# Kernel optimization log

Measured on AMD Instinct MI355X. Metric: run time of the kernel, lower is better.

## Reference

```python
import jax, jax.numpy as jnp
import numpy as np

B, C, N, K, COUT = 8, 128, 10000, 16, 256


def setup_inputs() -> dict:
    key = jax.random.key(0)
    ks = jax.random.split(key, 8)
    x = jax.random.normal(ks[0], (B, C, N, 1), dtype=jnp.float32)
    edge_index = jax.random.randint(ks[1], (2, B, N, K), 0, N)
    s1 = 1.0 / np.sqrt(C)
    W1 = jax.random.uniform(ks[2], (C, C), jnp.float32, -s1, s1)   # nn1 1x1 conv weight
    b1 = jax.random.uniform(ks[3], (C,), jnp.float32, -s1, s1)
    Wp = jax.random.uniform(ks[4], (C, C), jnp.float32, -s1, s1)   # nn_pooling Linear
    bp = jax.random.uniform(ks[5], (C,), jnp.float32, -s1, s1)
    s2 = 1.0 / np.sqrt(2 * C)
    W2 = jax.random.uniform(ks[6], (COUT, 2 * C), jnp.float32, -s2, s2)  # nn2 1x1 conv
    b2 = jax.random.uniform(ks[7], (COUT,), jnp.float32, -s2, s2)
    return dict(x=x, edge_index=edge_index, W1=W1, b1=b1, Wp=Wp, bp=bp, W2=W2, b2=b2)


def reference(x, edge_index, W1, b1, Wp, bp, W2, b2):
    b, c, n, _ = x.shape
    k = edge_index.shape[-1]
    # nn1: 1x1 conv (channel mix) + ReLU -> [B,C,N,1]
    h = jax.nn.relu(jnp.einsum('bcns,dc->bdns', x, W1) + b1[None, :, None, None])
    # batched_index_select: gather neighbor features along vertex dim -> [B,C,N,K]
    hn = h[:, :, :, 0]                              # [B,C,N]
    idx = edge_index[0].reshape(b, 1, n * k)        # broadcast over C
    xj = jnp.take_along_axis(hn, idx, axis=2).reshape(b, c, n, k)
    # nn_pooling: Linear over channel dim + ReLU (transpose(1,3) in torch == act on C)
    xj = jax.nn.relu(jnp.einsum('bcnk,dc->bdnk', xj, Wp) + bp[None, :, None, None])
    # max-pool over neighbors, keepdim -> [B,C,N,1]
    xj = jnp.max(xj, axis=-1, keepdims=True)
    # concat along channels, nn2: 1x1 conv + ReLU -> [B,COUT,N,1]
    cat = jnp.concatenate([h, xj], axis=1)
    out = jax.nn.relu(jnp.einsum('bcns,dc->bdns', cat, W2) + b2[None, :, None, None])
    return out
```

## Files before the change

### kernel.cpp

```cpp
#include <hip/hip_runtime.h>

#define NODES 10000
#define BATCH 8
#define CH    128
#define KNB   16
#define CO    256

typedef __bf16 bf16x8 __attribute__((ext_vector_type(8)));
typedef float  f32x4  __attribute__((ext_vector_type(4)));

__device__ __forceinline__ unsigned short f2bf(float f) {
  unsigned u = __float_as_uint(f);
  u = (u + 0x7FFFu + ((u >> 16) & 1u)) >> 16;
  return (unsigned short)u;
}

__device__ __forceinline__ unsigned pkmax(unsigned a, unsigned b) {
  unsigned d;
  asm("v_pk_max_u16 %0, %1, %2" : "=v"(d) : "v"(a), "v"(b));
  return d;
}
__device__ __forceinline__ uint4 pkmax4(uint4 a, uint4 b) {
  a.x = pkmax(a.x, b.x); a.y = pkmax(a.y, b.y);
  a.z = pkmax(a.z, b.z); a.w = pkmax(a.w, b.w);
  return a;
}
__device__ __forceinline__ bf16x8 asbf8(uint4 u) {
  union { uint4 u; bf16x8 b; } c; c.u = u; return c.b;
}

__device__ __forceinline__ void gload_lds16(const void* g, void* l) {
  __builtin_amdgcn_global_load_lds(
      (const __attribute__((address_space(1))) unsigned int*)g,
      (__attribute__((address_space(3))) unsigned int*)l, 16, 0, 0);
}

__device__ __forceinline__ void lds_barrier() {
  asm volatile("s_waitcnt lgkmcnt(0)" ::: "memory");
  __builtin_amdgcn_sched_barrier(0);
  __builtin_amdgcn_s_barrier();
}

__global__ __launch_bounds__(256) void prep(
    const float* __restrict__ W1, const float* __restrict__ Wp,
    const float* __restrict__ W2,
    unsigned short* __restrict__ W1b, unsigned short* __restrict__ Wpb,
    unsigned short* __restrict__ W2b)
{
  int i = blockIdx.x * 256 + threadIdx.x;
  const float* src; unsigned short* dst; int off;
  if (i < 4096)      { src = W1; dst = W1b; off = i; }
  else if (i < 8192) { src = Wp; dst = Wpb; off = i - 4096; }
  else               { src = W2; dst = W2b; off = i - 8192; }
  float4 v = ((const float4*)src)[off];
  ushort4 o;
  o.x = f2bf(v.x); o.y = f2bf(v.y); o.z = f2bf(v.z); o.w = f2bf(v.w);
  ((ushort4*)dst)[off] = o;
}

__global__ __launch_bounds__(256) void prep_x(
    const float* __restrict__ x, unsigned short* __restrict__ x_t)
{
  const int b  = blockIdx.y;
  const int n0 = blockIdx.x * 64;
  const int t  = threadIdx.x;
  const size_t nb = (size_t)b * NODES;

  __shared__ __align__(16) unsigned short Bt[64 * 128];
  char* BtB = (char*)Bt;

  const float* X = x + (size_t)b * CH * NODES;
#pragma unroll
  for (int rep = 0; rep < 4; ++rep) {
    int flat = t + rep * 256;
    int c2 = flat >> 4, n4 = flat & 15;
    int c  = c2 * 2;
    int gn = n0 + n4 * 4;
    float4 a0 = make_float4(0.f,0.f,0.f,0.f), a1 = a0;
    if (gn < NODES) {
      a0 = *(const float4*)(X + (size_t)c * NODES + gn);
      a1 = *(const float4*)(X + (size_t)(c + 1) * NODES + gn);
    }
    float v0[4] = {a0.x, a0.y, a0.z, a0.w};
    float v1[4] = {a1.x, a1.y, a1.z, a1.w};
#pragma unroll
    for (int i = 0; i < 4; ++i) {
      int nn = n4 * 4 + i;
      unsigned pk = (unsigned)f2bf(v0[i]) | ((unsigned)f2bf(v1[i]) << 16);
      int phys = nn * 256 + (((c2 >> 2) ^ (nn & 7)) << 4) + ((c2 & 3) << 2);
      *(unsigned*)(BtB + phys) = pk;
    }
  }
  __syncthreads();

  {
    int nl = t >> 2;
    int gn = n0 + nl;
#pragma unroll
    for (int rep = 0; rep < 4; ++rep) {
      int g = (t & 3) + rep * 4;
      int phys = nl * 256 + ((g ^ (nl & 7)) << 4);
      uint4 v = *(const uint4*)(BtB + phys);
      if (gn < NODES)
        *(uint4*)((char*)x_t + (nb + (size_t)gn) * 256 + g * 16) = v;
    }
  }
}

__device__ __forceinline__ void hz_stage(
    unsigned short* buf, const unsigned short* __restrict__ x_t,
    size_t nb, int n0, int w, int lane)
{
#pragma unroll
  for (int rep = 0; rep < 4; ++rep) {
    const int row0 = w * 16 + rep * 4;
    const int nl = row0 + (lane >> 4);
    const int c  = lane & 15;
    const int l  = c ^ (nl & 7);
    int gn = n0 + nl; if (gn > NODES - 1) gn = NODES - 1;
    const unsigned short* src = x_t + (nb + (size_t)gn) * CH + l * 8;
    gload_lds16(src, (char*)buf + row0 * 256);
  }
  __builtin_amdgcn_sched_barrier(0);
}

__device__ __forceinline__ void hz_compute(
    const unsigned short* buf, unsigned short* Ht, unsigned short* Zt,
    const uint4 (&af)[4][4], const uint4 (&af2)[4][4],
    const float* __restrict__ b1, const float* __restrict__ bp,
    unsigned short* __restrict__ h_t, unsigned short* __restrict__ z_t,
    size_t nb, int n0, int t, int w, int lm, int q)
{
  const char* BtB = (const char*)buf;
  char* HtB = (char*)Ht;
  char* ZtB = (char*)Zt;
  const int d0  = (w & 1) * 64;
  const int nbw = (w >> 1) * 32;

  f32x4 acc[4][2];
#pragma unroll
  for (int dt = 0; dt < 4; ++dt)
#pragma unroll
    for (int nt = 0; nt < 2; ++nt) acc[dt][nt] = (f32x4){0.f,0.f,0.f,0.f};

#pragma unroll
  for (int kt = 0; kt < 4; ++kt)
#pragma unroll
    for (int nt = 0; nt < 2; ++nt) {
      int nl = nbw + nt * 16 + lm;
      int chunk = kt * 4 + q;
      int phys = nl * 256 + ((chunk ^ (nl & 7)) << 4);
      bf16x8 bb = asbf8(*(const uint4*)(BtB + phys));
#pragma unroll
      for (int dt = 0; dt < 4; ++dt)
        acc[dt][nt] = __builtin_amdgcn_mfma_f32_16x16x32_bf16(
            asbf8(af[dt][kt]), bb, acc[dt][nt], 0, 0, 0);
    }

#pragma unroll
  for (int dt = 0; dt < 4; ++dt) {
    int dbase = d0 + dt * 16 + q * 4;
    float4 bi = *(const float4*)(b1 + dbase);
    float bv[4] = {bi.x, bi.y, bi.z, bi.w};
#pragma unroll
    for (int nt = 0; nt < 2; ++nt) {
      int nl = nbw + nt * 16 + lm;
      ushort4 o;
      o.x = f2bf(fmaxf(acc[dt][nt][0] + bv[0], 0.f));
      o.y = f2bf(fmaxf(acc[dt][nt][1] + bv[1], 0.f));
      o.z = f2bf(fmaxf(acc[dt][nt][2] + bv[2], 0.f));
      o.w = f2bf(fmaxf(acc[dt][nt][3] + bv[3], 0.f));
      int chunk = dbase >> 3;
      int phys  = nl * 256 + ((chunk ^ (nl & 7)) << 4) + ((q & 1) << 3);
      *(ushort4*)(HtB + phys) = o;
    }
  }

  lds_barrier();

  {
    int nl = t >> 2;
    int gn = n0 + nl;
#pragma unroll
    for (int rep = 0; rep < 4; ++rep) {
      int g = (t & 3) + rep * 4;
      int phys = nl * 256 + ((g ^ (nl & 7)) << 4);
      uint4 v = *(const uint4*)(HtB + phys);
      if (gn < NODES)
        *(uint4*)((char*)h_t + (nb + (size_t)gn) * 256 + g * 16) = v;
    }
  }

#pragma unroll
  for (int dt = 0; dt < 4; ++dt)
#pragma unroll
    for (int nt = 0; nt < 2; ++nt) acc[dt][nt] = (f32x4){0.f,0.f,0.f,0.f};

#pragma unroll
  for (int kt = 0; kt < 4; ++kt)
#pragma unroll
    for (int nt = 0; nt < 2; ++nt) {
      int nl = nbw + nt * 16 + lm;
      int chunk = kt * 4 + q;
      int phys = nl * 256 + ((chunk ^ (nl & 7)) << 4);
      bf16x8 bb = asbf8(*(const uint4*)(HtB + phys));
#pragma unroll
      for (int dt = 0; dt < 4; ++dt)
        acc[dt][nt] = __builtin_amdgcn_mfma_f32_16x16x32_bf16(
            asbf8(af2[dt][kt]), bb, acc[dt][nt], 0, 0, 0);
    }

#pragma unroll
  for (int dt = 0; dt < 4; ++dt) {
    int dbase = d0 + dt * 16 + q * 4;
    float4 bi = *(const float4*)(bp + dbase);
    float bv[4] = {bi.x, bi.y, bi.z, bi.w};
#pragma unroll
    for (int nt = 0; nt < 2; ++nt) {
      int nl = nbw + nt * 16 + lm;
      ushort4 o;
      o.x = f2bf(fmaxf(acc[dt][nt][0] + bv[0], 0.f));
      o.y = f2bf(fmaxf(acc[dt][nt][1] + bv[1], 0.f));
      o.z = f2bf(fmaxf(acc[dt][nt][2] + bv[2], 0.f));
      o.w = f2bf(fmaxf(acc[dt][nt][3] + bv[3], 0.f));
      int chunk = dbase >> 3;
      int phys  = nl * 256 + ((chunk ^ (nl & 7)) << 4) + ((q & 1) << 3);
      *(ushort4*)(ZtB + phys) = o;
    }
  }

  lds_barrier();

  {
    int nl = t >> 2;
    int gn = n0 + nl;
#pragma unroll
    for (int rep = 0; rep < 4; ++rep) {
      int g = (t & 3) + rep * 4;
      int phys = nl * 256 + ((g ^ (nl & 7)) << 4);
      uint4 v = *(const uint4*)(ZtB + phys);
      if (gn < NODES)
        *(uint4*)((char*)z_t + (nb + (size_t)gn) * 256 + g * 16) = v;
    }
  }
}

__global__ __launch_bounds__(256) void fused_hz(
    const unsigned short* __restrict__ W1b, const float* __restrict__ b1,
    const unsigned short* __restrict__ Wpb, const float* __restrict__ bp,
    const unsigned short* __restrict__ x_t,
    unsigned short* __restrict__ h_t, unsigned short* __restrict__ z_t)
{
  const int bid = blockIdx.x;
  const int b   = bid & 7;
  const int g   = bid >> 3;
  const int t   = threadIdx.x;
  const int lane = t & 63, w = t >> 6;
  const int lm = lane & 15, q = lane >> 4;
  const size_t nb = (size_t)b * NODES;

  __shared__ __align__(16) unsigned short bufA[64 * 128];
  __shared__ __align__(16) unsigned short bufB[64 * 128];
  __shared__ __align__(16) unsigned short Ht[64 * 128];
  __shared__ __align__(16) unsigned short Zt[64 * 128];

  const int d0 = (w & 1) * 64;

  uint4 af[4][4], af2[4][4];
#pragma unroll
  for (int dt = 0; dt < 4; ++dt)
#pragma unroll
    for (int kt = 0; kt < 4; ++kt) {
      af[dt][kt]  = *(const uint4*)(W1b + (d0 + dt*16 + lm) * CH + kt*32 + q*8);
      af2[dt][kt] = *(const uint4*)(Wpb + (d0 + dt*16 + lm) * CH + kt*32 + q*8);
    }

  const int n0_0 = g * 64;
  const int n0_1 = (g + 64) * 64;
  const int n0_2 = (g + 128) * 64;
  const bool has2 = (g + 128) < 157;

  hz_stage(bufA, x_t, nb, n0_0, w, lane);
  asm volatile("s_waitcnt vmcnt(0) lgkmcnt(0)" ::: "memory");
  __builtin_amdgcn_sched_barrier(0);
  __builtin_amdgcn_s_barrier();

  hz_stage(bufB, x_t, nb, n0_1, w, lane);
  hz_compute(bufA, Ht, Zt, af, af2, b1, bp, h_t, z_t, nb, n0_0, t, w, lm, q);
  asm volatile("s_waitcnt vmcnt(8) lgkmcnt(0)" ::: "memory");
  __builtin_amdgcn_sched_barrier(0);
  __builtin_amdgcn_s_barrier();

  if (has2) {
    hz_stage(bufA, x_t, nb, n0_2, w, lane);
    hz_compute(bufB, Ht, Zt, af, af2, b1, bp, h_t, z_t, nb, n0_1, t, w, lm, q);
    asm volatile("s_waitcnt vmcnt(8) lgkmcnt(0)" ::: "memory");
    __builtin_amdgcn_sched_barrier(0);
    __builtin_amdgcn_s_barrier();
    hz_compute(bufA, Ht, Zt, af, af2, b1, bp, h_t, z_t, nb, n0_2, t, w, lm, q);
  } else {
    hz_compute(bufB, Ht, Zt, af, af2, b1, bp, h_t, z_t, nb, n0_1, t, w, lm, q);
  }
}

__global__ __launch_bounds__(256) void gmax_kernel(
    const unsigned short* __restrict__ z_t, const int* __restrict__ e0,
    unsigned short* __restrict__ zm)
{
  const int bid = blockIdx.x;
  const int b   = bid & 7;
  const int n0  = (bid >> 3) * 64;
  const int t   = threadIdx.x;
  const int nl  = t >> 2, c = t & 3;
  const int gn  = n0 + nl;
  if (gn >= NODES) return;

  const int* ip = e0 + ((size_t)b * NODES + gn) * KNB;
  int4 iv0 = *(const int4*)(ip);
  int4 iv1 = *(const int4*)(ip + 4);
  int4 iv2 = *(const int4*)(ip + 8);
  int4 iv3 = *(const int4*)(ip + 12);
  int idx[16] = {iv0.x, iv0.y, iv0.z, iv0.w,
                 iv1.x, iv1.y, iv1.z, iv1.w,
                 iv2.x, iv2.y, iv2.z, iv2.w,
                 iv3.x, iv3.y, iv3.z, iv3.w};

  const char* Z = (const char*)(z_t + (size_t)b * NODES * CH) + c * 16;
  uint4 m[4];
#pragma unroll
  for (int cg = 0; cg < 4; ++cg) m[cg] = make_uint4(0u, 0u, 0u, 0u);

#pragma unroll
  for (int k = 0; k < KNB; ++k) {
    const char* p = Z + (size_t)idx[k] * (CH * 2);
#pragma unroll
    for (int cg = 0; cg < 4; ++cg)
      m[cg] = pkmax4(m[cg], *(const uint4*)(p + cg * 64));
  }

  char* O = (char*)(zm + ((size_t)b * NODES + gn) * CH) + c * 16;
#pragma unroll
  for (int cg = 0; cg < 4; ++cg)
    *(uint4*)(O + cg * 64) = m[cg];
}

__device__ __forceinline__ void og_stage(
    unsigned short* buf, const unsigned short* __restrict__ h_t,
    const unsigned short* __restrict__ zm, size_t nb, int n0, int w, int lane)
{
#pragma unroll
  for (int rep = 0; rep < 8; ++rep) {
    const int row0 = w * 2 + rep * 8;
    const int nl = row0 + (lane >> 5);
    const int l  = (lane & 31) ^ (nl & 7);
    int gn = n0 + nl; if (gn > NODES - 1) gn = NODES - 1;
    const unsigned short* src = (l < 16)
        ? h_t + (nb + (size_t)gn) * CH + l * 8
        : zm  + (nb + (size_t)gn) * CH + (l - 16) * 8;
    gload_lds16(src, (char*)buf + row0 * 512);
  }
  __builtin_amdgcn_sched_barrier(0);
}

__device__ __forceinline__ void og_mfma(
    f32x4 (&acc)[4][4], const unsigned short* buf,
    const uint4 (&af)[8][4], int lm, int q)
{
  const char* catB = (const char*)buf;
#pragma unroll
  for (int dt = 0; dt < 4; ++dt)
#pragma unroll
    for (int nt = 0; nt < 4; ++nt) acc[dt][nt] = (f32x4){0.f, 0.f, 0.f, 0.f};
#pragma unroll
  for (int kt = 0; kt < 8; ++kt)
#pragma unroll
    for (int nt = 0; nt < 4; ++nt) {
      int nl = nt * 16 + lm;
      int chunk = kt * 4 + q;
      int phys = nl * 512 + ((chunk ^ (nl & 7)) << 4);
      bf16x8 bb = asbf8(*(const uint4*)(catB + phys));
#pragma unroll
      for (int dt = 0; dt < 4; ++dt)
        acc[dt][nt] = __builtin_amdgcn_mfma_f32_16x16x32_bf16(
            asbf8(af[kt][dt]), bb, acc[dt][nt], 0, 0, 0);
    }
}

__device__ __forceinline__ void og_epi(
    const f32x4 (&acc)[4][4], const float* __restrict__ b2,
    float* __restrict__ out, int b, int n0, int w, int lm, int q)
{
  const int d0 = w * 64;
#pragma unroll
  for (int dt = 0; dt < 4; ++dt) {
    int dbase = d0 + dt * 16 + q * 4;
    float4 bi = *(const float4*)(b2 + dbase);
    float bv[4] = {bi.x, bi.y, bi.z, bi.w};
#pragma unroll
    for (int nt = 0; nt < 4; ++nt) {
      int gn = n0 + nt * 16 + lm;
      if (gn < NODES) {
        float* op = out + ((size_t)(b * CO + dbase) * NODES) + gn;
#pragma unroll
        for (int r = 0; r < 4; ++r)
          op[(size_t)r * NODES] = fmaxf(acc[dt][nt][r] + bv[r], 0.f);
      }
    }
  }
}

__global__ __launch_bounds__(256) void out_gemm(
    const unsigned short* __restrict__ h_t, const unsigned short* __restrict__ zm,
    const unsigned short* __restrict__ W2b, const float* __restrict__ b2,
    float* __restrict__ out)
{
  const int bid = blockIdx.x;
  const int b   = bid & 7;
  const int g   = bid >> 3;
  const int t   = threadIdx.x;
  const int lane = t & 63, w = t >> 6;
  const int lm = lane & 15, q = lane >> 4;
  const size_t nb = (size_t)b * NODES;

  __shared__ __align__(16) unsigned short bufA[64 * 256];
  __shared__ __align__(16) unsigned short bufB[64 * 256];

  const int d0 = w * 64;
  uint4 af[8][4];
#pragma unroll
  for (int kt = 0; kt < 8; ++kt)
#pragma unroll
    for (int dt = 0; dt < 4; ++dt)
      af[kt][dt] = *(const uint4*)(W2b + (d0 + dt*16 + lm) * CO + kt*32 + q*8);

  const int n0_0 = g * 64;
  const int n0_1 = (g + 64) * 64;
  const int n0_2 = (g + 128) * 64;
  const bool has2 = (g + 128) < 157;

  f32x4 acc[4][4];

  og_stage(bufA, h_t, zm, nb, n0_0, w, lane);
  asm volatile("s_waitcnt vmcnt(0) lgkmcnt(0)" ::: "memory");
  __builtin_amdgcn_sched_barrier(0);
  __builtin_amdgcn_s_barrier();

  og_stage(bufB, h_t, zm, nb, n0_1, w, lane);
  og_mfma(acc, bufA, af, lm, q);
  asm volatile("s_waitcnt vmcnt(0) lgkmcnt(0)" ::: "memory");
  __builtin_amdgcn_sched_barrier(0);
  __builtin_amdgcn_s_barrier();

  if (has2) {
    og_stage(bufA, h_t, zm, nb, n0_2, w, lane);
    og_epi(acc, b2, out, b, n0_0, w, lm, q);
    og_mfma(acc, bufB, af, lm, q);
    asm volatile("s_waitcnt vmcnt(56) lgkmcnt(0)" ::: "memory");
    __builtin_amdgcn_sched_barrier(0);
    __builtin_amdgcn_s_barrier();
    og_epi(acc, b2, out, b, n0_1, w, lm, q);
    og_mfma(acc, bufA, af, lm, q);
    og_epi(acc, b2, out, b, n0_2, w, lm, q);
  } else {
    og_epi(acc, b2, out, b, n0_0, w, lm, q);
    og_mfma(acc, bufB, af, lm, q);
    og_epi(acc, b2, out, b, n0_1, w, lm, q);
  }
}

extern "C" void kernel_launch(void* const* d_in, const int* in_sizes, int n_in,
                              void* d_out, int out_size, void* d_ws, size_t ws_size,
                              hipStream_t stream) {
  const float* x  = (const float*)d_in[0];
  const int*   ei = (const int*)d_in[1];
  const float* W1 = (const float*)d_in[2];
  const float* b1 = (const float*)d_in[3];
  const float* Wp = (const float*)d_in[4];
  const float* bp = (const float*)d_in[5];
  const float* W2 = (const float*)d_in[6];
  const float* b2 = (const float*)d_in[7];
  float* out = (float*)d_out;

  unsigned short* ws  = (unsigned short*)d_ws;
  unsigned short* h_t = ws;
  unsigned short* z_t = h_t + (size_t)BATCH * NODES * CH;
  unsigned short* W1b = z_t + (size_t)BATCH * NODES * CH;
  unsigned short* Wpb = W1b + CH * CH;
  unsigned short* W2b = Wpb + CH * CH;
  unsigned short* zm  = W2b + CO * 2 * CH;
  unsigned short* x_t = zm  + (size_t)BATCH * NODES * CH;

  prep<<<96, 256, 0, stream>>>(W1, Wp, W2, W1b, Wpb, W2b);

  const int NT = (NODES + 63) / 64;
  prep_x<<<dim3(NT, BATCH), 256, 0, stream>>>(x, x_t);
  fused_hz<<<512, 256, 0, stream>>>(W1b, b1, Wpb, bp, x_t, h_t, z_t);
  gmax_kernel<<<BATCH * NT, 256, 0, stream>>>(z_t, ei, zm);
  out_gemm<<<512, 256, 0, stream>>>(h_t, zm, W2b, b2, out);
}
```

Baseline: 196.1 us.

## Fuse x transpose/bf16 conversion into fused_hz, removing prep_x kernel

Drops the separate prep_x kernel that wrote a transposed bf16 copy of x to global memory. fused_hz now loads fp32 x directly into registers, converts to bf16 and writes the swizzled LDS tile itself, with the next tile's load overlapped with compute on the current one. This removes one kernel launch and a full global write and read of the transposed x. In exchange each block holds more registers for the prefetched fp32 data, and the LDS writes happen in the compute loop instead of through async direct-to-LDS loads.

```diff
diff --git a/kernel.cpp b/kernel.cpp
--- a/kernel.cpp
+++ b/kernel.cpp
@@ -58,70 +58,41 @@
   ((ushort4*)dst)[off] = o;
 }
 
-__global__ __launch_bounds__(256) void prep_x(
-    const float* __restrict__ x, unsigned short* __restrict__ x_t)
-{
-  const int b  = blockIdx.y;
-  const int n0 = blockIdx.x * 64;
-  const int t  = threadIdx.x;
-  const size_t nb = (size_t)b * NODES;
-
-  __shared__ __align__(16) unsigned short Bt[64 * 128];
-  char* BtB = (char*)Bt;
-
-  const float* X = x + (size_t)b * CH * NODES;
+__device__ __forceinline__ void hz_load_x(
+    f32x4 (&xa)[4][2], const float* __restrict__ X, int n0, int t)
+{
 #pragma unroll
   for (int rep = 0; rep < 4; ++rep) {
     int flat = t + rep * 256;
     int c2 = flat >> 4, n4 = flat & 15;
     int c  = c2 * 2;
     int gn = n0 + n4 * 4;
-    float4 a0 = make_float4(0.f,0.f,0.f,0.f), a1 = a0;
+    f32x4 a0 = (f32x4){0.f,0.f,0.f,0.f}, a1 = a0;
     if (gn < NODES) {
-      a0 = *(const float4*)(X + (size_t)c * NODES + gn);
-      a1 = *(const float4*)(X + (size_t)(c + 1) * NODES + gn);
-    }
-    float v0[4] = {a0.x, a0.y, a0.z, a0.w};
-    float v1[4] = {a1.x, a1.y, a1.z, a1.w};
+      a0 = *(const f32x4*)(X + (size_t)c * NODES + gn);
+      a1 = *(const f32x4*)(X + (size_t)(c + 1) * NODES + gn);
+    }
+    xa[rep][0] = a0; xa[rep][1] = a1;
+  }
+}
+
+__device__ __forceinline__ void hz_write_buf(
+    const f32x4 (&xa)[4][2], unsigned short* buf, int t)
+{
+  char* BtB = (char*)buf;
+#pragma unroll
+  for (int rep = 0; rep < 4; ++rep) {
+    int flat = t + rep * 256;
+    int c2 = flat >> 4, n4 = flat & 15;
 #pragma unroll
     for (int i = 0; i < 4; ++i) {
       int nn = n4 * 4 + i;
-      unsigned pk = (unsigned)f2bf(v0[i]) | ((unsigned)f2bf(v1[i]) << 16);
+      unsigned pk = (unsigned)f2bf(xa[rep][0][i])
+                  | ((unsigned)f2bf(xa[rep][1][i]) << 16);
       int phys = nn * 256 + (((c2 >> 2) ^ (nn & 7)) << 4) + ((c2 & 3) << 2);
       *(unsigned*)(BtB + phys) = pk;
     }
   }
-  __syncthreads();
-
-  {
-    int nl = t >> 2;
-    int gn = n0 + nl;
-#pragma unroll
-    for (int rep = 0; rep < 4; ++rep) {
-      int g = (t & 3) + rep * 4;
-      int phys = nl * 256 + ((g ^ (nl & 7)) << 4);
-      uint4 v = *(const uint4*)(BtB + phys);
-      if (gn < NODES)
-        *(uint4*)((char*)x_t + (nb + (size_t)gn) * 256 + g * 16) = v;
-    }
-  }
-}
-
-__device__ __forceinline__ void hz_stage(
-    unsigned short* buf, const unsigned short* __restrict__ x_t,
-    size_t nb, int n0, int w, int lane)
-{
-#pragma unroll
-  for (int rep = 0; rep < 4; ++rep) {
-    const int row0 = w * 16 + rep * 4;
-    const int nl = row0 + (lane >> 4);
-    const int c  = lane & 15;
-    const int l  = c ^ (nl & 7);
-    int gn = n0 + nl; if (gn > NODES - 1) gn = NODES - 1;
-    const unsigned short* src = x_t + (nb + (size_t)gn) * CH + l * 8;
-    gload_lds16(src, (char*)buf + row0 * 256);
-  }
-  __builtin_amdgcn_sched_barrier(0);
 }
 
 __device__ __forceinline__ void hz_compute(
@@ -248,7 +219,7 @@
 __global__ __launch_bounds__(256) void fused_hz(
     const unsigned short* __restrict__ W1b, const float* __restrict__ b1,
     const unsigned short* __restrict__ Wpb, const float* __restrict__ bp,
-    const unsigned short* __restrict__ x_t,
+    const float* __restrict__ x,
     unsigned short* __restrict__ h_t, unsigned short* __restrict__ z_t)
 {
   const int bid = blockIdx.x;
@@ -258,6 +229,7 @@
   const int lane = t & 63, w = t >> 6;
   const int lm = lane & 15, q = lane >> 4;
   const size_t nb = (size_t)b * NODES;
+  const float* X = x + (size_t)b * CH * NODES;
 
   __shared__ __align__(16) unsigned short bufA[64 * 128];
   __shared__ __align__(16) unsigned short bufB[64 * 128];
@@ -280,23 +252,22 @@
   const int n0_2 = (g + 128) * 64;
   const bool has2 = (g + 128) < 157;
 
-  hz_stage(bufA, x_t, nb, n0_0, w, lane);
-  asm volatile("s_waitcnt vmcnt(0) lgkmcnt(0)" ::: "memory");
-  __builtin_amdgcn_sched_barrier(0);
-  __builtin_amdgcn_s_barrier();
-
-  hz_stage(bufB, x_t, nb, n0_1, w, lane);
+  f32x4 xa[4][2];
+
+  hz_load_x(xa, X, n0_0, t);
+  hz_write_buf(xa, bufA, t);
+  __syncthreads();
+
+  hz_load_x(xa, X, n0_1, t);
   hz_compute(bufA, Ht, Zt, af, af2, b1, bp, h_t, z_t, nb, n0_0, t, w, lm, q);
-  asm volatile("s_waitcnt vmcnt(8) lgkmcnt(0)" ::: "memory");
-  __builtin_amdgcn_sched_barrier(0);
-  __builtin_amdgcn_s_barrier();
+  hz_write_buf(xa, bufB, t);
+  __syncthreads();
 
   if (has2) {
-    hz_stage(bufA, x_t, nb, n0_2, w, lane);
+    hz_load_x(xa, X, n0_2, t);
     hz_compute(bufB, Ht, Zt, af, af2, b1, bp, h_t, z_t, nb, n0_1, t, w, lm, q);
-    asm volatile("s_waitcnt vmcnt(8) lgkmcnt(0)" ::: "memory");
-    __builtin_amdgcn_sched_barrier(0);
-    __builtin_amdgcn_s_barrier();
+    hz_write_buf(xa, bufA, t);
+    __syncthreads();
     hz_compute(bufA, Ht, Zt, af, af2, b1, bp, h_t, z_t, nb, n0_2, t, w, lm, q);
   } else {
     hz_compute(bufB, Ht, Zt, af, af2, b1, bp, h_t, z_t, nb, n0_1, t, w, lm, q);
@@ -488,13 +459,11 @@
   unsigned short* Wpb = W1b + CH * CH;
   unsigned short* W2b = Wpb + CH * CH;
   unsigned short* zm  = W2b + CO * 2 * CH;
-  unsigned short* x_t = zm  + (size_t)BATCH * NODES * CH;
 
   prep<<<96, 256, 0, stream>>>(W1, Wp, W2, W1b, Wpb, W2b);
 
   const int NT = (NODES + 63) / 64;
-  prep_x<<<dim3(NT, BATCH), 256, 0, stream>>>(x, x_t);
-  fused_hz<<<512, 256, 0, stream>>>(W1b, b1, Wpb, bp, x_t, h_t, z_t);
+  fused_hz<<<512, 256, 0, stream>>>(W1b, b1, Wpb, bp, x, h_t, z_t);
   gmax_kernel<<<BATCH * NT, 256, 0, stream>>>(z_t, ei, zm);
   out_gemm<<<512, 256, 0, stream>>>(h_t, zm, W2b, b2, out);
 }
```

Measured after the change: 195.0 us (median of 2 runs). No clear change (-0.6%).
